# Optimization experiments

Hardware: AMD Instinct MI355X
Metric: run time of the kernel (lower is better)

Reference implementation:

```python
import jax, jax.numpy as jnp
import numpy as np

B, T, C = 4, 2048, 1024
H, D = 16, 64  # num_heads, head_dim
WINDOW = 256


def setup_inputs() -> dict:
    key = jax.random.key(0)
    k_x, k_qkv, k_proj, k_qb, k_pb = jax.random.split(key, 5)
    x = jax.random.normal(k_x, (B, T, C), dtype=jnp.float32)
    # xavier-uniform-ish init for qkv weight (as in _reset_parameters)
    lim_qkv = float(np.sqrt(6.0 / (C + 3 * C)))
    qkv_w = jax.random.uniform(k_qkv, (3 * C, C), minval=-lim_qkv, maxval=lim_qkv, dtype=jnp.float32)
    qkv_b = jax.random.normal(k_qb, (3 * C,), dtype=jnp.float32) * 0.02
    lim_p = float(np.sqrt(1.0 / C))
    proj_w = jax.random.uniform(k_proj, (C, C), minval=-lim_p, maxval=lim_p, dtype=jnp.float32)
    proj_b = jax.random.normal(k_pb, (C,), dtype=jnp.float32) * 0.02
    # windowed causal mask: attend to j iff j <= i and i - j < WINDOW
    i = jnp.arange(T)[:, None]
    j = jnp.arange(T)[None, :]
    attn_mask = (j <= i) & (i - j < WINDOW)  # [T, T] bool
    return {"x": x, "attn_mask": attn_mask, "qkv_w": qkv_w, "qkv_b": qkv_b,
            "proj_w": proj_w, "proj_b": proj_b}


def reference(x, attn_mask, qkv_w, qkv_b, proj_w, proj_b):
    qkv = (x @ qkv_w.T + qkv_b).reshape(B, T, 3, H, D)
    qkv = jnp.transpose(qkv, (2, 0, 3, 1, 4))
    q, k, v = qkv[0], qkv[1], qkv[2]
    scale = 1.0 / jnp.sqrt(jnp.asarray(D, dtype=q.dtype))
    scores = jnp.einsum('bhqd,bhkd->bhqk', q, k) * scale  # [B,H,T,T]
    neg = jnp.asarray(jnp.finfo(scores.dtype).min, dtype=scores.dtype)
    scores = jnp.where(attn_mask[None, None], scores, neg)
    attn = jax.nn.softmax(scores, axis=-1)
    out = jnp.einsum('bhqk,bhkd->bhqd', attn, v)  # [B,H,T,D]
    out = jnp.transpose(out, (0, 2, 1, 3)).reshape(B, T, C)
    out = out @ proj_w.T + proj_b
    return out
```

## Files before the change

### kernel.cpp

```cpp
#include <hip/hip_runtime.h>

#define BB 4
#define TT 2048
#define CC 1024
#define HH 16
#define DD 64
#define WIN 256

typedef __attribute__((ext_vector_type(8))) short short8;
typedef __attribute__((ext_vector_type(4))) float floatx4;
typedef unsigned short u16;

typedef __attribute__((address_space(3))) void lds_void;
typedef const __attribute__((address_space(1))) void g_void;

__device__ __forceinline__ void gl_lds16(const u16* g, u16* l) {
    __builtin_amdgcn_global_load_lds((g_void*)g, (lds_void*)l, 16, 0, 0);
}

__device__ __forceinline__ float bf2f(u16 u) {
    union { unsigned int i; float f; } v; v.i = ((unsigned int)u) << 16; return v.f;
}
__device__ __forceinline__ u16 f2bf(float f) {
    union { float f; unsigned int i; } v; v.f = f;
    unsigned int x = v.i;
    x += ((x >> 16) & 1u) + 0x7FFFu;
    return (u16)(x >> 16);
}

__global__ void cvt_all(const float* __restrict__ x, const float* __restrict__ qw,
                        const float* __restrict__ pw,
                        u16* __restrict__ xb, u16* __restrict__ wb, u16* __restrict__ pwb) {
    int bid = blockIdx.x;
    const float* src; u16* dst; int off;
    if (bid < 4096)      { src = x;  dst = xb;  off = bid; }
    else if (bid < 5632) { src = qw; dst = wb;  off = bid - 4096; }
    else                 { src = pw; dst = pwb; off = bid - 5632; }
    int i = (off * 256 + (int)threadIdx.x) * 8;
    float4 a = *(const float4*)(src + i);
    float4 b = *(const float4*)(src + i + 4);
    u16 o[8] = { f2bf(a.x), f2bf(a.y), f2bf(a.z), f2bf(a.w),
                 f2bf(b.x), f2bf(b.y), f2bf(b.z), f2bf(b.w) };
    *(uint4*)(dst + i) = *(const uint4*)o;
}


#define STG(buf, kh, t) do { const int ko = (t) * 64 + (kh) * 32;            \
        gl_lds16(gA0 + ko, &lA[buf][kh][wave * 512]);                        \
        gl_lds16(gA1 + ko, &lA[buf][kh][4096 + wave * 512]);                 \
        gl_lds16(gB0 + ko, &lB[buf][kh][wave * 512]); } while (0)
#define LDAB(buf, kk) do { _Pragma("unroll")                                 \
        for (int i = 0; i < 4; ++i)                                          \
            af[i] = *(const short8*)&lA[buf][kk][(wm * 4 + i) * 512 + rdoff];\
        _Pragma("unroll")                                                    \
        for (int j = 0; j < 4; ++j)                                          \
            bf[j] = *(const short8*)&lB[buf][kk][(wn * 4 + j) * 512 + rdoff]; } while (0)
#define MM() do { __builtin_amdgcn_s_setprio(1); _Pragma("unroll")           \
        for (int i = 0; i < 4; ++i) { _Pragma("unroll")                      \
            for (int j = 0; j < 4; ++j)                                      \
                acc[i][j] = __builtin_amdgcn_mfma_f32_16x16x32_bf16(         \
                    af[i], bf[j], acc[i][j], 0, 0, 0); }                     \
        __builtin_amdgcn_s_setprio(0); } while (0)
#define BARX() do { asm volatile("" ::: "memory");                           \
        __builtin_amdgcn_s_barrier();                                        \
        asm volatile("" ::: "memory"); } while (0)
#define VM6() asm volatile("s_waitcnt vmcnt(6)" ::: "memory")

#define GEMM_BODY                                                            \
    const int K = CC;                                                        \
    __shared__ u16 lA[2][2][8192];                                           \
    __shared__ u16 lB[2][2][4096];                                           \
    const int tid = threadIdx.x;                                             \
    const int wave = tid >> 6, lane = tid & 63;                              \
    const int wm = wave >> 1, wn = wave & 1;                                 \
    const int quad = lane >> 4, l15 = lane & 15;                             \
    const int r0 = wave * 16 + (lane >> 2);                                  \
    const int r1 = r0 + 128;                                                 \
    const int c0 = (lane & 3) ^ ((r0 >> 1) & 3);                             \
    const u16* gA0 = Amat + (size_t)(bM + r0) * K + c0 * 8;                  \
    const u16* gA1 = Amat + (size_t)(bM + r1) * K + c0 * 8;                  \
    const u16* gB0 = Bw + (size_t)(bN + r0) * K + c0 * 8;                    \
    const int rdoff = l15 * 32 + ((quad ^ ((l15 >> 1) & 3)) * 8);            \
    floatx4 acc[4][4] = {};                                                  \
    STG(0, 0, 0); STG(0, 1, 0); STG(1, 0, 1);                                \
    VM6(); BARX();                                                           \
    for (int ii = 0; ii < 8; ++ii) {                                         \
        const int t0 = 2 * ii, t1 = t0 + 1;                                  \
        const int t2 = (t0 + 2 < 16) ? t0 + 2 : t0;                          \
        const int t3 = (t1 + 2 < 16) ? t1 + 2 : t1;                          \
        short8 af[4], bf[4];                                                 \
        LDAB(0, 0); STG(1, 1, t1); VM6(); BARX(); MM(); BARX();              \
        LDAB(0, 1); STG(0, 0, t2); VM6(); BARX(); MM(); BARX();              \
        LDAB(1, 0); STG(0, 1, t2); VM6(); BARX(); MM(); BARX();              \
        LDAB(1, 1); STG(1, 0, t3); VM6(); BARX(); MM(); BARX();              \
    }

__global__ __launch_bounds__(512, 2) void gemm_qkv(
    const u16* __restrict__ Amat, const u16* __restrict__ Bw,
    const float* __restrict__ bias,
    u16* __restrict__ Qb, u16* __restrict__ Kb, u16* __restrict__ Vb)
{
    const int raw = blockIdx.x;
    const int swz = (raw & 7) * 96 + (raw >> 3);
    const int bN = (swz >> 5) * 128;
    const int bM = (swz & 31) * 256;

    GEMM_BODY

#pragma unroll
    for (int mf = 0; mf < 4; ++mf)
#pragma unroll
        for (int nf = 0; nf < 4; ++nf) {
            int col = bN + wn * 64 + nf * 16 + l15;
            float bv = bias[col];
            int which = col >> 10, rem = col & 1023;
            int h = rem >> 6, d = rem & 63;
            u16* dst = which == 0 ? Qb : (which == 1 ? Kb : Vb);
#pragma unroll
            for (int rg = 0; rg < 4; ++rg) {
                int row = bM + wm * 64 + mf * 16 + quad * 4 + rg;
                int b = row >> 11, t = row & 2047;
                float v = acc[mf][nf][rg] + bv;
                dst[(((size_t)(b * HH + h)) * TT + t) * DD + d] = f2bf(v);
            }
        }
}

__global__ __launch_bounds__(512, 2) void gemm_proj(
    const u16* __restrict__ Amat, const u16* __restrict__ Bw,
    const float* __restrict__ bias, float* __restrict__ Out)
{
    const int raw = blockIdx.x;
    const int swz = (raw & 7) * 32 + (raw >> 3);
    const int bN = (swz >> 5) * 128;
    const int bM = (swz & 31) * 256;

    GEMM_BODY

#pragma unroll
    for (int mf = 0; mf < 4; ++mf)
#pragma unroll
        for (int nf = 0; nf < 4; ++nf) {
            int col = bN + wn * 64 + nf * 16 + l15;
            float bv = bias[col];
#pragma unroll
            for (int rg = 0; rg < 4; ++rg) {
                int row = bM + wm * 64 + mf * 16 + quad * 4 + rg;
                Out[(size_t)row * CC + col] = acc[mf][nf][rg] + bv;
            }
        }
}

#undef STG
#undef LDAB
#undef MM
#undef BARX
#undef VM6
#undef GEMM_BODY

__global__ __launch_bounds__(256) void attn_mfma(
    const u16* __restrict__ Qb, const u16* __restrict__ Kb, const u16* __restrict__ Vb,
    u16* __restrict__ Y)
{
    __shared__ u16 Ks[64][72];
    __shared__ u16 Vt[64][72];
    __shared__ u16 Ps[4][16][72];

    const int tid = threadIdx.x;
    const int wave = tid >> 6, lane = tid & 63;
    const int quad = lane >> 4, l15 = lane & 15;
    const int q0 = blockIdx.x * 64;
    const int bh = blockIdx.y;
    const int b = bh >> 4, h = bh & 15;
    const u16* Qp = Qb + (size_t)bh * TT * DD;
    const u16* Kp = Kb + (size_t)bh * TT * DD;
    const u16* Vp = Vb + (size_t)bh * TT * DD;
    const int qw = q0 + wave * 16;

    short8 qf[2];
    qf[0] = *(const short8*)&Qp[(size_t)(qw + l15) * DD + quad * 8];
    qf[1] = *(const short8*)&Qp[(size_t)(qw + l15) * DD + 32 + quad * 8];

    float m_i[4] = { -1e30f, -1e30f, -1e30f, -1e30f };
    float l_i[4] = { 0.f, 0.f, 0.f, 0.f };
    floatx4 Oacc[4] = {};

    const int kb = (q0 >= WIN) ? (q0 - WIN) : 0;
    for (int j0 = kb; j0 < q0 + 64; j0 += 64) {
        __syncthreads();
#pragma unroll
        for (int it = 0; it < 2; ++it) {
            int slot = tid + it * 256;
            int j = slot >> 3, c8 = (slot & 7) << 3;
            *(uint4*)&Ks[j][c8] = *(const uint4*)&Kp[(size_t)(j0 + j) * DD + c8];
        }
#pragma unroll
        for (int it = 0; it < 2; ++it) {
            int slot = tid + it * 256;
            int j = slot >> 3, d0 = (slot & 7) << 3;
            uint4 raw = *(const uint4*)&Vp[(size_t)(j0 + j) * DD + d0];
            const u16* u = (const u16*)&raw;
#pragma unroll
            for (int i = 0; i < 8; ++i) {
                int d = d0 + i;
                int col = (((j >> 3) ^ (d >> 3)) << 3) + (j & 7);
                Vt[d][col] = u[i];
            }
        }
        __syncthreads();

        floatx4 Sacc[4] = {};
#pragma unroll
        for (int nt = 0; nt < 4; ++nt) {
            short8 kf0 = *(const short8*)&Ks[nt * 16 + l15][quad * 8];
            short8 kf1 = *(const short8*)&Ks[nt * 16 + l15][32 + quad * 8];
            Sacc[nt] = __builtin_amdgcn_mfma_f32_16x16x32_bf16(qf[0], kf0, Sacc[nt], 0, 0, 0);
            Sacc[nt] = __builtin_amdgcn_mfma_f32_16x16x32_bf16(qf[1], kf1, Sacc[nt], 0, 0, 0);
        }

        float mc[4] = { -1e30f, -1e30f, -1e30f, -1e30f };
#pragma unroll
        for (int nt = 0; nt < 4; ++nt)
#pragma unroll
            for (int r = 0; r < 4; ++r) {
                int q = qw + quad * 4 + r;
                int j = j0 + nt * 16 + l15;
                float s = (j <= q && (q - j) < WIN) ? Sacc[nt][r] * 0.125f : -1e30f;
                Sacc[nt][r] = s;
                mc[r] = fmaxf(mc[r], s);
            }
#pragma unroll
        for (int m = 1; m < 16; m <<= 1)
#pragma unroll
            for (int r = 0; r < 4; ++r) mc[r] = fmaxf(mc[r], __shfl_xor(mc[r], m, 64));

        float alpha[4];
#pragma unroll
        for (int r = 0; r < 4; ++r) {
            float mn = fmaxf(m_i[r], mc[r]);
            alpha[r] = __expf(m_i[r] - mn);
            m_i[r] = mn;
        }
        float rs[4] = { 0.f, 0.f, 0.f, 0.f };
#pragma unroll
        for (int nt = 0; nt < 4; ++nt)
#pragma unroll
            for (int r = 0; r < 4; ++r) {
                float s = Sacc[nt][r];
                float p = (s > -1e29f) ? __expf(s - m_i[r]) : 0.f;
                Sacc[nt][r] = p;
                rs[r] += p;
            }
#pragma unroll
        for (int m = 1; m < 16; m <<= 1)
#pragma unroll
            for (int r = 0; r < 4; ++r) rs[r] += __shfl_xor(rs[r], m, 64);
#pragma unroll
        for (int r = 0; r < 4; ++r) l_i[r] = l_i[r] * alpha[r] + rs[r];
#pragma unroll
        for (int dt = 0; dt < 4; ++dt)
#pragma unroll
            for (int r = 0; r < 4; ++r) Oacc[dt][r] *= alpha[r];

#pragma unroll
        for (int nt = 0; nt < 4; ++nt)
#pragma unroll
            for (int r = 0; r < 4; ++r)
                Ps[wave][quad * 4 + r][nt * 16 + l15] = f2bf(Sacc[nt][r]);

#pragma unroll
        for (int ks = 0; ks < 2; ++ks) {
            short8 pf = *(const short8*)&Ps[wave][l15][ks * 32 + quad * 8];
#pragma unroll
            for (int dt = 0; dt < 4; ++dt) {
                int d = dt * 16 + l15;
                int col = (((ks * 4 + quad) ^ (d >> 3)) << 3);
                short8 vf = *(const short8*)&Vt[d][col];
                Oacc[dt] = __builtin_amdgcn_mfma_f32_16x16x32_bf16(pf, vf, Oacc[dt], 0, 0, 0);
            }
        }
    }

    float inv[4];
#pragma unroll
    for (int r = 0; r < 4; ++r) inv[r] = 1.f / l_i[r];
#pragma unroll
    for (int dt = 0; dt < 4; ++dt)
#pragma unroll
        for (int r = 0; r < 4; ++r) {
            int t = qw + quad * 4 + r;
            int d = dt * 16 + l15;
            Y[((size_t)b * TT + t) * CC + h * DD + d] = f2bf(Oacc[dt][r] * inv[r]);
        }
}

extern "C" void kernel_launch(void* const* d_in, const int* in_sizes, int n_in,
                              void* d_out, int out_size, void* d_ws, size_t ws_size,
                              hipStream_t stream) {
    const float* x      = (const float*)d_in[0];
    const float* qkv_w  = (const float*)d_in[2];
    const float* qkv_b  = (const float*)d_in[3];
    const float* proj_w = (const float*)d_in[4];
    const float* proj_b = (const float*)d_in[5];
    float* out = (float*)d_out;

    u16* xb  = (u16*)d_ws;
    u16* wb  = xb  + (size_t)8192 * 1024;
    u16* pwb = wb  + (size_t)3072 * 1024;
    u16* Qb  = pwb + (size_t)1024 * 1024;
    u16* Kb  = Qb  + (size_t)64 * 2048 * 64;
    u16* Vb  = Kb  + (size_t)64 * 2048 * 64;
    u16* Yb  = Vb  + (size_t)64 * 2048 * 64;

    cvt_all<<<6144, 256, 0, stream>>>(x, qkv_w, proj_w, xb, wb, pwb);
    gemm_qkv<<<768, 512, 0, stream>>>(xb, wb, qkv_b, Qb, Kb, Vb);
    attn_mfma<<<dim3(TT / 64, BB * HH), 256, 0, stream>>>(Qb, Kb, Vb, Yb);
    gemm_proj<<<256, 512, 0, stream>>>(Yb, pwb, proj_b, out);
}
```

Baseline: 263.2 us.

## Deepen GEMM LDS pipeline to six-stage ring and remap block tiles per XCD

Replaces the double-buffered, two-half-tile GEMM loop with a six-slot ring of 32-wide K stages. Five stages are kept in flight through global_load_lds, with waits on vmcnt(12), and the 32-iteration loop is fully unrolled. The block-to-tile mapping also changes so that each XCD owns four consecutive M tiles across all N tiles, aiming for better L2 reuse of the activation rows. The cost is a larger LDS footprint of about 144KB per block, which rules out two blocks per CU, and more unrolled code.

```diff
diff --git a/kernel.cpp b/kernel.cpp
--- a/kernel.cpp
+++ b/kernel.cpp
@@ -45,16 +45,16 @@
 }
 
 
-#define STG(buf, kh, t) do { const int ko = (t) * 64 + (kh) * 32;            \
-        gl_lds16(gA0 + ko, &lA[buf][kh][wave * 512]);                        \
-        gl_lds16(gA1 + ko, &lA[buf][kh][4096 + wave * 512]);                 \
-        gl_lds16(gB0 + ko, &lB[buf][kh][wave * 512]); } while (0)
-#define LDAB(buf, kk) do { _Pragma("unroll")                                 \
+#define STG(s, t) do { const int ko = (t) * 32;                              \
+        gl_lds16(gA0 + ko, &lA[s][wave * 512]);                              \
+        gl_lds16(gA1 + ko, &lA[s][4096 + wave * 512]);                       \
+        gl_lds16(gB0 + ko, &lB[s][wave * 512]); } while (0)
+#define LDAB(s) do { _Pragma("unroll")                                       \
         for (int i = 0; i < 4; ++i)                                          \
-            af[i] = *(const short8*)&lA[buf][kk][(wm * 4 + i) * 512 + rdoff];\
+            af[i] = *(const short8*)&lA[s][(wm * 4 + i) * 512 + rdoff];      \
         _Pragma("unroll")                                                    \
         for (int j = 0; j < 4; ++j)                                          \
-            bf[j] = *(const short8*)&lB[buf][kk][(wn * 4 + j) * 512 + rdoff]; } while (0)
+            bf[j] = *(const short8*)&lB[s][(wn * 4 + j) * 512 + rdoff]; } while (0)
 #define MM() do { __builtin_amdgcn_s_setprio(1); _Pragma("unroll")           \
         for (int i = 0; i < 4; ++i) { _Pragma("unroll")                      \
             for (int j = 0; j < 4; ++j)                                      \
@@ -64,12 +64,12 @@
 #define BARX() do { asm volatile("" ::: "memory");                           \
         __builtin_amdgcn_s_barrier();                                        \
         asm volatile("" ::: "memory"); } while (0)
-#define VM6() asm volatile("s_waitcnt vmcnt(6)" ::: "memory")
+#define VM12() asm volatile("s_waitcnt vmcnt(12)" ::: "memory")
 
 #define GEMM_BODY                                                            \
     const int K = CC;                                                        \
-    __shared__ u16 lA[2][2][8192];                                           \
-    __shared__ u16 lB[2][2][4096];                                           \
+    __shared__ u16 lA[6][8192];                                              \
+    __shared__ u16 lB[6][4096];                                              \
     const int tid = threadIdx.x;                                             \
     const int wave = tid >> 6, lane = tid & 63;                              \
     const int wm = wave >> 1, wn = wave & 1;                                 \
@@ -82,17 +82,14 @@
     const u16* gB0 = Bw + (size_t)(bN + r0) * K + c0 * 8;                    \
     const int rdoff = l15 * 32 + ((quad ^ ((l15 >> 1) & 3)) * 8);            \
     floatx4 acc[4][4] = {};                                                  \
-    STG(0, 0, 0); STG(0, 1, 0); STG(1, 0, 1);                                \
-    VM6(); BARX();                                                           \
-    for (int ii = 0; ii < 8; ++ii) {                                         \
-        const int t0 = 2 * ii, t1 = t0 + 1;                                  \
-        const int t2 = (t0 + 2 < 16) ? t0 + 2 : t0;                          \
-        const int t3 = (t1 + 2 < 16) ? t1 + 2 : t1;                          \
+    STG(0, 0); STG(1, 1); STG(2, 2); STG(3, 3); STG(4, 4);                   \
+    VM12(); BARX();                                                          \
+    _Pragma("unroll")                                                        \
+    for (int P = 0; P < 32; ++P) {                                           \
         short8 af[4], bf[4];                                                 \
-        LDAB(0, 0); STG(1, 1, t1); VM6(); BARX(); MM(); BARX();              \
-        LDAB(0, 1); STG(0, 0, t2); VM6(); BARX(); MM(); BARX();              \
-        LDAB(1, 0); STG(0, 1, t2); VM6(); BARX(); MM(); BARX();              \
-        LDAB(1, 1); STG(1, 0, t3); VM6(); BARX(); MM(); BARX();              \
+        LDAB(P % 6);                                                         \
+        STG((P + 5) % 6, (P + 5 < 32) ? (P + 5) : (P - 1));                  \
+        VM12(); BARX(); MM(); BARX();                                        \
     }
 
 __global__ __launch_bounds__(512, 2) void gemm_qkv(
@@ -101,9 +98,10 @@
     u16* __restrict__ Qb, u16* __restrict__ Kb, u16* __restrict__ Vb)
 {
     const int raw = blockIdx.x;
-    const int swz = (raw & 7) * 96 + (raw >> 3);
-    const int bN = (swz >> 5) * 128;
-    const int bM = (swz & 31) * 256;
+    const int xcd = raw & 7;
+    const int l   = raw >> 3;
+    const int bM  = (xcd * 4 + (l & 3)) * 256;
+    const int bN  = (l >> 2) * 128;
 
     GEMM_BODY
 
@@ -131,9 +129,10 @@
     const float* __restrict__ bias, float* __restrict__ Out)
 {
     const int raw = blockIdx.x;
-    const int swz = (raw & 7) * 32 + (raw >> 3);
-    const int bN = (swz >> 5) * 128;
-    const int bM = (swz & 31) * 256;
+    const int xcd = raw & 7;
+    const int l   = raw >> 3;
+    const int bM  = (xcd * 4 + (l & 3)) * 256;
+    const int bN  = (l >> 2) * 128;
 
     GEMM_BODY
 
@@ -155,7 +154,7 @@
 #undef LDAB
 #undef MM
 #undef BARX
-#undef VM6
+#undef VM12
 #undef GEMM_BODY
 
 __global__ __launch_bounds__(256) void attn_mfma(
```

After: 243.2 us. -7.6%, faster.
